# Optimization experiments

Measured on AMD Instinct MI355X. Metric: run time of the kernel, lower is better.

Reference implementation:

```python
import jax, jax.numpy as jnp
import numpy as np

B, T, D, DI, K, M, H, HD, L, VOCAB = 8, 512, 256, 512, 4, 2, 4, 64, 2, 272


def rmsnorm(x, w, eps=1e-6):
    return x * jax.lax.rsqrt(jnp.mean(x * x, axis=-1, keepdims=True) + eps) * w


def rotate_half(x):
    x1, x2 = x[..., ::2], x[..., 1::2]
    return jnp.stack([-x2, x1], axis=-1).reshape(x.shape)


def causal_conv(x, w, b):
    # x: [B,T,C], w: [C,K] depthwise causal conv, then silu
    y = jax.lax.conv_general_dilated(
        x.transpose(0, 2, 1), w[:, None, :],
        window_strides=(1,), padding=[(K - 1, 0)],
        feature_group_count=x.shape[-1])
    return jax.nn.silu(y.transpose(0, 2, 1) + b)


def delta_memory(x, Wv, Wg, Wb, Wa, A_log, dt_bias, Wblend, Wout):
    # x: [B,T,D]; per-timestep delta-rule fast-weight update with decay + key rotation
    Bv, Tn, Dm = x.shape
    vals = (x @ Wv).reshape(Bv, Tn, M, H, HD)
    gate = jax.nn.sigmoid(x @ Wg)                                   # [B,T,H]
    beta = jax.nn.sigmoid(jnp.einsum('btd,mdh->btmh', x, Wb))       # [B,T,M,H]
    alpha = jnp.einsum('btd,mdh->btmh', x, Wa) + dt_bias            # [B,T,M,H]
    decay = jnp.exp(-jnp.exp(A_log)[None, None] * jax.nn.softplus(alpha))
    blend = jax.nn.softmax((x @ Wblend).reshape(Bv, Tn, H, M), axis=-1)
    rk0 = x.reshape(Bv, Tn, H, HD)
    rk0 = rk0 / jnp.maximum(jnp.linalg.norm(rk0, axis=-1, keepdims=True), 1e-12)
    rks = [rk0]
    for _ in range(M - 1):
        rks.append(rotate_half(rks[-1]))
    rks = jnp.stack(rks, axis=2)                                    # [B,T,M,H,d]
    wks = jnp.pad(rks[:, :-1], ((0, 0), (1, 0), (0, 0), (0, 0), (0, 0)))  # shifted keys

    def step(S, inp):
        v, wk, rk, bt, dc, bl, g = inp
        S = S * dc[..., None, None]                                  # [B,M,H,d,d]
        pred = jnp.einsum('bmhdk,bmhd->bmhk', S, wk)
        err = (v - pred) * bt[..., None]
        S = S + wk[..., None] * err[..., None, :]                    # outer-product write
        read = jnp.einsum('bmhdk,bmhd->bmhk', S, rk)
        o = jnp.einsum('bhm,bmhk->bhk', bl, read) * g[..., None]
        return S, o

    tf = lambda a: jnp.moveaxis(a, 1, 0)
    xs = (tf(vals), tf(wks), tf(rks), tf(beta), tf(decay), tf(blend), tf(gate))
    S0 = jnp.zeros((Bv, M, H, HD, HD), x.dtype)
    _, o = jax.lax.scan(step, S0, xs)                                # [T,B,H,d]
    o = jnp.moveaxis(o, 0, 1).reshape(Bv, Tn, Dm)
    return x + o @ Wout


def setup_inputs():
    key = jax.random.key(0)
    ks = jax.random.split(key, 16)
    n = lambda k, shape, sc=0.02: jax.random.normal(k, shape, jnp.float32) * sc
    return {
        'ids': jax.random.randint(ks[0], (B, T), 0, VOCAB, jnp.int32),
        'emb': n(ks[1], (VOCAB, D)),
        'norm_w': jnp.ones((L, D), jnp.float32),
        'W_up': n(ks[2], (L, D, DI)),
        'W_gate': n(ks[3], (L, D, DI)),
        'W_down': n(ks[4], (L, DI, D)),
        'conv_w': n(ks[5], (L, DI, K), 0.1),
        'conv_b': jnp.zeros((L, DI), jnp.float32),
        'Wv': n(ks[6], (L, D, M * D)),
        'Wg': n(ks[7], (L, D, H)),
        'Wb': n(ks[8], (L, M, D, H)),
        'Wa': n(ks[9], (L, M, D, H)),
        'A_log': n(ks[10], (L, M, H), 0.5),
        'dt_bias': n(ks[11], (L, M, H), 0.5),
        'Wblend': n(ks[12], (L, D, H * M)),
        'Wout': n(ks[13], (L, D, D)),
        'final_norm_w': jnp.ones((D,), jnp.float32),
    }


def reference(ids, emb, norm_w, W_up, W_gate, W_down, conv_w, conv_b,
              Wv, Wg, Wb, Wa, A_log, dt_bias, Wblend, Wout, final_norm_w):
    x = emb[ids]
    for l in range(L):
        nx = rmsnorm(x, norm_w[l])
        h = causal_conv(nx @ W_up[l], conv_w[l], conv_b[l])
        out = (jax.nn.silu(nx @ W_gate[l]) * h) @ W_down[l]
        out = delta_memory(out, Wv[l], Wg[l], Wb[l], Wa[l],
                           A_log[l], dt_bias[l], Wblend[l], Wout[l])
        x = x + out
    return rmsnorm(x, final_norm_w) @ emb.T  # tied head
```

## Files before the change

kernel.cpp:

```cpp
#include <hip/hip_runtime.h>
#include <math.h>

#define BB 8
#define TT 512
#define DD 256
#define DIM 512
#define KW 4
#define MM 2
#define HH 4
#define HDIM 64
#define LL 2
#define VV 272

typedef __attribute__((ext_vector_type(8))) short bf16x8;
typedef __attribute__((ext_vector_type(4))) float f32x4;

__device__ __forceinline__ float sigf(float x){ return 1.f/(1.f+__expf(-x)); }
__device__ __forceinline__ float siluf(float x){ return x/(1.f+__expf(-x)); }

__device__ __forceinline__ unsigned short f2bf(float f){
  unsigned int u = __float_as_uint(f);
  unsigned int r = (u + 0x7FFFu + ((u >> 16) & 1u)) >> 16;
  return (unsigned short)r;
}
__device__ __forceinline__ float bf2f(unsigned short s){
  return __uint_as_float(((unsigned int)s) << 16);
}

__device__ __forceinline__ float xor1_add(float x){
  int y = __builtin_amdgcn_update_dpp(0, __float_as_int(x), 0xB1, 0xF, 0xF, true);
  return x + __int_as_float(y);
}
__device__ __forceinline__ float xor2_add(float x){
  int y = __builtin_amdgcn_update_dpp(0, __float_as_int(x), 0x4E, 0xF, 0xF, true);
  return x + __int_as_float(y);
}
__device__ __forceinline__ float ror4_add(float x){
  int y = __builtin_amdgcn_update_dpp(0, __float_as_int(x), 0x124, 0xF, 0xF, true);
  return x + __int_as_float(y);
}
__device__ __forceinline__ float ror8_add(float x){
  int y = __builtin_amdgcn_update_dpp(0, __float_as_int(x), 0x128, 0xF, 0xF, true);
  return x + __int_as_float(y);
}

__device__ __forceinline__ void gl_lds16(const void* g, void* l){
  __builtin_amdgcn_global_load_lds(
      (const __attribute__((address_space(1))) unsigned int*)g,
      (__attribute__((address_space(3))) unsigned int*)l,
      16, 0, 0);
}

#define LWB 589824
__global__ void k_cvt(const float* __restrict__ Wup, const float* __restrict__ Wgate,
                      const float* __restrict__ Wdown, const float* __restrict__ Wv,
                      const float* __restrict__ Wout, const float* __restrict__ emb,
                      unsigned short* __restrict__ wbf){
  int idx = blockIdx.x*256 + threadIdx.x;
  if (idx >= 2*LWB + VV*DD) return;
  float v;
  if (idx < 2*LWB){
    int l = (idx >= LWB) ? 1 : 0;
    int local = idx - l*LWB;
    if (local < 131072){ int n = local>>8, k = local&255;
      v = Wup[(size_t)l*131072 + k*DIM + n]; }
    else if (local < 262144){ local -= 131072; int n = local>>8, k = local&255;
      v = Wgate[(size_t)l*131072 + k*DIM + n]; }
    else if (local < 393216){ local -= 262144; int n = local>>9, k = local&511;
      v = Wdown[(size_t)l*131072 + k*DD + n]; }
    else if (local < 524288){ local -= 393216; int n = local>>8, k = local&255;
      v = Wv[(size_t)l*131072 + k*DIM + n]; }
    else { local -= 524288; int n = local>>8, k = local&255;
      v = Wout[(size_t)l*65536 + k*DD + n]; }
  } else {
    v = emb[idx - 2*LWB];
  }
  wbf[idx] = f2bf(v);
}

__global__ void __launch_bounds__(256) k_embed_norm(const int* __restrict__ ids,
                                                    const float* __restrict__ emb,
                                                    const float* __restrict__ w,
                                                    float* __restrict__ x,
                                                    unsigned short* __restrict__ out){
  const int wv = threadIdx.x >> 6, l = threadIdx.x & 63;
  const int row = blockIdx.x*4 + wv;
  float4 v = *(const float4*)&emb[(size_t)ids[row]*DD + l*4];
  *(float4*)&x[(size_t)row*DD + l*4] = v;
  float ss = v.x*v.x + v.y*v.y + v.z*v.z + v.w*v.w;
  #pragma unroll
  for (int o = 32; o > 0; o >>= 1) ss += __shfl_xor(ss, o, 64);
  float sc = rsqrtf(ss*(1.f/DD) + 1e-6f);
  float4 wvv = *(const float4*)&w[l*4];
  ushort4 r;
  r.x = f2bf(v.x*sc*wvv.x); r.y = f2bf(v.y*sc*wvv.y);
  r.z = f2bf(v.z*sc*wvv.z); r.w = f2bf(v.w*sc*wvv.w);
  *(ushort4*)&out[(size_t)row*DD + l*4] = r;
}

__global__ void __launch_bounds__(256) k_rmsnorm(const float* __restrict__ in,
                                                 const float* __restrict__ w,
                                                 unsigned short* __restrict__ out){
  const int wv = threadIdx.x >> 6, l = threadIdx.x & 63;
  const int row = blockIdx.x*4 + wv;
  float4 v = *(const float4*)&in[(size_t)row*DD + l*4];
  float ss = v.x*v.x + v.y*v.y + v.z*v.z + v.w*v.w;
  #pragma unroll
  for (int o = 32; o > 0; o >>= 1) ss += __shfl_xor(ss, o, 64);
  float sc = rsqrtf(ss*(1.f/DD) + 1e-6f);
  float4 wvv = *(const float4*)&w[l*4];
  ushort4 r;
  r.x = f2bf(v.x*sc*wvv.x); r.y = f2bf(v.y*sc*wvv.y);
  r.z = f2bf(v.z*sc*wvv.z); r.w = f2bf(v.w*sc*wvv.w);
  *(ushort4*)&out[(size_t)row*DD + l*4] = r;
}

template<int MODE>
__global__ void __launch_bounds__(256) k_gemm64(const unsigned short* __restrict__ A,
                                                const unsigned short* __restrict__ Bt,
                                                float* __restrict__ Cf,
                                                unsigned short* __restrict__ Cb,
                                                int N, int K){
  __shared__ unsigned short as[64][72];
  __shared__ unsigned short bs[64][72];
  const int tid = threadIdx.x;
  const int w = tid >> 6, l = tid & 63;
  const int m0 = blockIdx.y*64, n0 = blockIdx.x*64;
  const int ar = tid >> 2, ac = (tid & 3)*16;
  f32x4 acc[4] = {};
  for (int k0 = 0; k0 < K; k0 += 64){
    { const bf16x8* src = (const bf16x8*)&A[(size_t)(m0+ar)*K + k0 + ac];
      *(bf16x8*)&as[ar][ac]   = src[0];
      *(bf16x8*)&as[ar][ac+8] = src[1];
    }
    { int n = n0 + ar;
      bf16x8 z; z = (bf16x8)(short)0;
      bf16x8 b0 = z, b1 = z;
      if (n < N){
        const bf16x8* src = (const bf16x8*)&Bt[(size_t)n*K + k0 + ac];
        b0 = src[0]; b1 = src[1];
      }
      *(bf16x8*)&bs[ar][ac]   = b0;
      *(bf16x8*)&bs[ar][ac+8] = b1;
    }
    __syncthreads();
    const int mr = w*16 + (l & 15);
    const int kb = (l >> 4)*8;
    #pragma unroll
    for (int kc2 = 0; kc2 < 2; ++kc2){
      bf16x8 af = *(const bf16x8*)&as[mr][kc2*32 + kb];
      #pragma unroll
      for (int nt = 0; nt < 4; ++nt){
        bf16x8 bfr = *(const bf16x8*)&bs[nt*16 + (l & 15)][kc2*32 + kb];
        acc[nt] = __builtin_amdgcn_mfma_f32_16x16x32_bf16(af, bfr, acc[nt], 0, 0, 0);
      }
    }
    __syncthreads();
  }
  #pragma unroll
  for (int nt = 0; nt < 4; ++nt){
    int col = n0 + nt*16 + (l & 15);
    if (col < N){
      #pragma unroll
      for (int r = 0; r < 4; ++r){
        int row = m0 + w*16 + (l >> 4)*4 + r;
        if (MODE == 0 || MODE == 2) Cf[(size_t)row*N + col] = acc[nt][r];
        if (MODE == 1 || MODE == 2) Cb[(size_t)row*N + col] = f2bf(acc[nt][r]);
      }
    }
  }
}

template<int MODE>
__global__ void __launch_bounds__(256) k_gemm128(const unsigned short* __restrict__ A,
                                                 const unsigned short* __restrict__ Bt,
                                                 float* __restrict__ Cf,
                                                 unsigned short* __restrict__ Cb,
                                                 int N, int K){
  __shared__ unsigned short as[128][72];
  __shared__ unsigned short bs[64][72];
  const int tid = threadIdx.x;
  const int w = tid >> 6, l = tid & 63;
  const int m0 = blockIdx.y*128, n0 = blockIdx.x*64;
  const int ar = tid >> 1, ac = (tid & 1)*32;
  const int br = tid >> 2, bc = (tid & 3)*16;
  f32x4 acc[2][4] = {};
  for (int k0 = 0; k0 < K; k0 += 64){
    { const bf16x8* src = (const bf16x8*)&A[(size_t)(m0+ar)*K + k0 + ac];
      *(bf16x8*)&as[ar][ac]    = src[0];
      *(bf16x8*)&as[ar][ac+8]  = src[1];
      *(bf16x8*)&as[ar][ac+16] = src[2];
      *(bf16x8*)&as[ar][ac+24] = src[3];
    }
    { int n = n0 + br;
      bf16x8 z; z = (bf16x8)(short)0;
      bf16x8 b0 = z, b1 = z;
      if (n < N){
        const bf16x8* s = (const bf16x8*)&Bt[(size_t)n*K + k0 + bc];
        b0 = s[0]; b1 = s[1];
      }
      *(bf16x8*)&bs[br][bc]   = b0;
      *(bf16x8*)&bs[br][bc+8] = b1;
    }
    __syncthreads();
    const int lr = l & 15, kb = (l >> 4)*8;
    #pragma unroll
    for (int kc2 = 0; kc2 < 2; ++kc2){
      bf16x8 af0 = *(const bf16x8*)&as[w*32 + lr][kc2*32 + kb];
      bf16x8 af1 = *(const bf16x8*)&as[w*32 + 16 + lr][kc2*32 + kb];
      #pragma unroll
      for (int nt = 0; nt < 4; ++nt){
        bf16x8 bfr = *(const bf16x8*)&bs[nt*16 + lr][kc2*32 + kb];
        acc[0][nt] = __builtin_amdgcn_mfma_f32_16x16x32_bf16(af0, bfr, acc[0][nt], 0, 0, 0);
        acc[1][nt] = __builtin_amdgcn_mfma_f32_16x16x32_bf16(af1, bfr, acc[1][nt], 0, 0, 0);
      }
    }
    __syncthreads();
  }
  const int lr = l & 15;
  #pragma unroll
  for (int mt = 0; mt < 2; ++mt){
    #pragma unroll
    for (int nt = 0; nt < 4; ++nt){
      int col = n0 + nt*16 + lr;
      if (col < N){
        #pragma unroll
        for (int r = 0; r < 4; ++r){
          int row = m0 + w*32 + mt*16 + (l >> 4)*4 + r;
          if (MODE == 0 || MODE == 2) Cf[(size_t)row*N + col] = acc[mt][nt][r];
          if (MODE == 1 || MODE == 2) Cb[(size_t)row*N + col] = f2bf(acc[mt][nt][r]);
        }
      }
    }
  }
}

__global__ void __launch_bounds__(256) k_gemm_up(const unsigned short* __restrict__ A,
                                                 const unsigned short* __restrict__ But,
                                                 const unsigned short* __restrict__ Bgt,
                                                 unsigned short* __restrict__ Cu,
                                                 unsigned short* __restrict__ Cg){
  __shared__ unsigned short as[128][72];
  __shared__ unsigned short bu[64][72];
  __shared__ unsigned short bg[64][72];
  const int tid = threadIdx.x;
  const int w = tid >> 6, l = tid & 63;
  const int m0 = blockIdx.y*128, n0 = blockIdx.x*64;
  const int ar = tid >> 1, ac = (tid & 1)*32;
  const int br = tid >> 2, bc = (tid & 3)*16;
  f32x4 accu[2][4] = {}; f32x4 accg[2][4] = {};
  for (int k0 = 0; k0 < DD; k0 += 64){
    { const bf16x8* src = (const bf16x8*)&A[(size_t)(m0+ar)*DD + k0 + ac];
      *(bf16x8*)&as[ar][ac]    = src[0];
      *(bf16x8*)&as[ar][ac+8]  = src[1];
      *(bf16x8*)&as[ar][ac+16] = src[2];
      *(bf16x8*)&as[ar][ac+24] = src[3];
    }
    { const bf16x8* s0 = (const bf16x8*)&But[(size_t)(n0+br)*DD + k0 + bc];
      *(bf16x8*)&bu[br][bc]   = s0[0];
      *(bf16x8*)&bu[br][bc+8] = s0[1];
      const bf16x8* s1 = (const bf16x8*)&Bgt[(size_t)(n0+br)*DD + k0 + bc];
      *(bf16x8*)&bg[br][bc]   = s1[0];
      *(bf16x8*)&bg[br][bc+8] = s1[1];
    }
    __syncthreads();
    const int lr = l & 15, kb = (l >> 4)*8;
    #pragma unroll
    for (int kc2 = 0; kc2 < 2; ++kc2){
      bf16x8 af0 = *(const bf16x8*)&as[w*32 + lr][kc2*32 + kb];
      bf16x8 af1 = *(const bf16x8*)&as[w*32 + 16 + lr][kc2*32 + kb];
      #pragma unroll
      for (int nt = 0; nt < 4; ++nt){
        bf16x8 b0 = *(const bf16x8*)&bu[nt*16 + lr][kc2*32 + kb];
        accu[0][nt] = __builtin_amdgcn_mfma_f32_16x16x32_bf16(af0, b0, accu[0][nt], 0, 0, 0);
        accu[1][nt] = __builtin_amdgcn_mfma_f32_16x16x32_bf16(af1, b0, accu[1][nt], 0, 0, 0);
        bf16x8 b1 = *(const bf16x8*)&bg[nt*16 + lr][kc2*32 + kb];
        accg[0][nt] = __builtin_amdgcn_mfma_f32_16x16x32_bf16(af0, b1, accg[0][nt], 0, 0, 0);
        accg[1][nt] = __builtin_amdgcn_mfma_f32_16x16x32_bf16(af1, b1, accg[1][nt], 0, 0, 0);
      }
    }
    __syncthreads();
  }
  const int lr = l & 15;
  #pragma unroll
  for (int mt = 0; mt < 2; ++mt){
    #pragma unroll
    for (int nt = 0; nt < 4; ++nt){
      int col = n0 + nt*16 + lr;
      #pragma unroll
      for (int r = 0; r < 4; ++r){
        int row = m0 + w*32 + mt*16 + (l >> 4)*4 + r;
        Cu[(size_t)row*DIM + col] = f2bf(accu[mt][nt][r]);
        Cg[(size_t)row*DIM + col] = f2bf(accg[mt][nt][r]);
      }
    }
  }
}

__global__ void __launch_bounds__(256) k_gemm_wout(const float* __restrict__ p0,
                                                   const float* __restrict__ p1,
                                                   const unsigned short* __restrict__ Bt,
                                                   const float* __restrict__ y,
                                                   float* __restrict__ x){
  __shared__ unsigned short as[64][72];
  __shared__ unsigned short bs[64][72];
  const int tid = threadIdx.x;
  const int w = tid >> 6, l = tid & 63;
  const int m0 = blockIdx.y*64, n0 = blockIdx.x*64;
  const int ar = tid >> 2, ac = (tid & 3)*16;
  f32x4 acc[4] = {};
  for (int k0 = 0; k0 < DD; k0 += 64){
    #pragma unroll
    for (int j = 0; j < 4; ++j){
      size_t off = (size_t)(m0+ar)*DD + k0 + ac + j*4;
      float4 a = *(const float4*)&p0[off];
      float4 b = *(const float4*)&p1[off];
      a.x += b.x; a.y += b.y; a.z += b.z; a.w += b.w;
      ushort4 u = make_ushort4(f2bf(a.x), f2bf(a.y), f2bf(a.z), f2bf(a.w));
      *(ushort4*)&as[ar][ac + j*4] = u;
    }
    { const bf16x8* src = (const bf16x8*)&Bt[(size_t)(n0+ar)*DD + k0 + ac];
      *(bf16x8*)&bs[ar][ac]   = src[0];
      *(bf16x8*)&bs[ar][ac+8] = src[1];
    }
    __syncthreads();
    const int mr = w*16 + (l & 15);
    const int kb = (l >> 4)*8;
    #pragma unroll
    for (int kc2 = 0; kc2 < 2; ++kc2){
      bf16x8 af = *(const bf16x8*)&as[mr][kc2*32 + kb];
      #pragma unroll
      for (int nt = 0; nt < 4; ++nt){
        bf16x8 bfr = *(const bf16x8*)&bs[nt*16 + (l & 15)][kc2*32 + kb];
        acc[nt] = __builtin_amdgcn_mfma_f32_16x16x32_bf16(af, bfr, acc[nt], 0, 0, 0);
      }
    }
    __syncthreads();
  }
  #pragma unroll
  for (int nt = 0; nt < 4; ++nt){
    int col = n0 + nt*16 + (l & 15);
    #pragma unroll
    for (int r = 0; r < 4; ++r){
      int row = m0 + w*16 + (l >> 4)*4 + r;
      size_t off = (size_t)row*DD + col;
      x[off] = x[off] + y[off] + acc[nt][r];
    }
  }
}

__global__ void k_conv(const unsigned short* __restrict__ u,
                       const unsigned short* __restrict__ g,
                       const float* __restrict__ cw, const float* __restrict__ cb,
                       unsigned short* __restrict__ hh){
  int i8 = blockIdx.x*256 + threadIdx.x;
  int cg = i8 & 63;
  int bt = i8 >> 6;
  int t  = bt & (TT-1);
  int c0 = cg*8;
  float acc[8];
  { float4 b0 = *(const float4*)&cb[c0];
    float4 b1 = *(const float4*)&cb[c0+4];
    acc[0]=b0.x; acc[1]=b0.y; acc[2]=b0.z; acc[3]=b0.w;
    acc[4]=b1.x; acc[5]=b1.y; acc[6]=b1.z; acc[7]=b1.w; }
  float wts[8][4];
  #pragma unroll
  for (int i = 0; i < 8; ++i) *(float4*)&wts[i][0] = *(const float4*)&cw[(c0+i)*KW];
  #pragma unroll
  for (int j = 0; j < KW; ++j){
    int dt_ = j - (KW-1);
    if (t + dt_ >= 0){
      bf16x8 uv = *(const bf16x8*)&u[(size_t)(bt + dt_)*DIM + c0];
      #pragma unroll
      for (int i = 0; i < 8; ++i)
        acc[i] = fmaf(bf2f((unsigned short)uv[i]), wts[i][j], acc[i]);
    }
  }
  bf16x8 gv = *(const bf16x8*)&g[(size_t)bt*DIM + c0];
  bf16x8 o;
  #pragma unroll
  for (int i = 0; i < 8; ++i){
    float h = siluf(acc[i]);
    o[i] = (short)f2bf(siluf(bf2f((unsigned short)gv[i])) * h);
  }
  *(bf16x8*)&hh[(size_t)bt*DIM + c0] = o;
}

__global__ void __launch_bounds__(256) k_fused(const float* __restrict__ y,
    const float* __restrict__ Wg, const float* __restrict__ Wb,
    const float* __restrict__ Wa, const float* __restrict__ Wbl,
    const float* __restrict__ A_log, const float* __restrict__ dtb,
    float* __restrict__ rkb, float* __restrict__ scal){
  __shared__ float s_y[4][260];
  __shared__ float s_p[4][32];
  const int wv = threadIdx.x >> 6, l = threadIdx.x & 63;
  const int row = blockIdx.x*4 + wv;

  float4 yv = *(const float4*)&y[(size_t)row*DD + l*4];
  *(float4*)&s_y[wv][l*4] = yv;

  float ss = yv.x*yv.x + yv.y*yv.y + yv.z*yv.z + yv.w*yv.w;
  ss = xor1_add(ss); ss = xor2_add(ss);
  ss = ror4_add(ss); ss = ror8_add(ss);
  float inv = 1.f / fmaxf(sqrtf(ss), 1e-12f);
  float4 rv; rv.x = yv.x*inv; rv.y = yv.y*inv; rv.z = yv.z*inv; rv.w = yv.w*inv;
  *(float4*)&rkb[(size_t)row*DD + l*4] = rv;

  __syncthreads();

  const int j = (l < 28) ? l : 27;
  const float* wp; int stride;
  if (j < 4){ wp = Wg + j; stride = HH; }
  else if (j < 12){ int m=(j-4)>>2, h=(j-4)&3; wp = Wb + (size_t)m*DD*HH + h; stride = HH; }
  else if (j < 20){ int m=(j-12)>>2, h=(j-12)&3; wp = Wa + (size_t)m*DD*HH + h; stride = HH; }
  else { wp = Wbl + (j-20); stride = HH*MM; }
  float a0=0.f,a1=0.f,a2=0.f,a3=0.f;
  #pragma unroll 4
  for (int k = 0; k < DD; k += 4){
    a0 = fmaf(s_y[wv][k+0], wp[(k+0)*stride], a0);
    a1 = fmaf(s_y[wv][k+1], wp[(k+1)*stride], a1);
    a2 = fmaf(s_y[wv][k+2], wp[(k+2)*stride], a2);
    a3 = fmaf(s_y[wv][k+3], wp[(k+3)*stride], a3);
  }
  if (l < 28) s_p[wv][l] = (a0+a1)+(a2+a3);

  __syncthreads();

  if (l < 8){
    int m = l >> 2, h = l & 3;
    float gs  = sigf(s_p[wv][h]);
    float btv = sigf(s_p[wv][4 + m*4 + h]);
    float sp  = s_p[wv][12 + m*4 + h] + dtb[m*HH + h];
    sp = (sp > 15.f) ? sp : log1pf(__expf(sp));
    float dc  = __expf(-__expf(A_log[m*HH + h]) * sp);
    float l0 = s_p[wv][20 + h*2], l1 = s_p[wv][20 + h*2 + 1];
    float mx = fmaxf(l0, l1);
    float e0 = __expf(l0-mx), e1 = __expf(l1-mx);
    float bl = (m ? e1 : e0) / (e0 + e1);
    float4 o; o.x = dc; o.y = btv; o.z = bl*gs; o.w = 0.f;
    *(float4*)&scal[((size_t)row*MM + m)*(HH*4) + h*4] = o;
  }
}


#define SSTEP(T_, WK, RK, PF, VB, SB) { \
  const float dc = SB.x, btv = SB.y, blg = SB.z; \
  const float v = VB; \
  { const int tn_ = ((T_)+2 < 64) ? (T_)+2 : 63; \
    PF = *(const float4*)&s_rk[p][tn_][dbase]; \
    VB = bf2f(s_v[p][tn_][vidx]); \
    SB = *(const float4*)&s_sc[p][tn_][0]; } \
  const float err = (v - dc*rrc)*btv; \
  float rr0=0.f, rr1=0.f; \
  { const float4 rp = WK; const float4 rc = RK; \
    float w0,w1,w2,w3,c0,c1,c2,c3; \
    if (ROT == 0){ w0=rp.x; w1=rp.y; w2=rp.z; w3=rp.w; c0=rc.x; c1=rc.y; c2=rc.z; c3=rc.w; } \
    else { w0=-rp.y; w1=rp.x; w2=-rp.w; w3=rp.z; c0=-rc.y; c1=rc.x; c2=-rc.w; c3=rc.z; } \
    S[0] = fmaf(S[0], dc, w0*err); rr0 = fmaf(S[0], c0, rr0); \
    S[1] = fmaf(S[1], dc, w1*err); rr1 = fmaf(S[1], c1, rr1); \
    S[2] = fmaf(S[2], dc, w2*err); rr0 = fmaf(S[2], c2, rr0); \
    S[3] = fmaf(S[3], dc, w3*err); rr1 = fmaf(S[3], c3, rr1); } \
  float rr = rr0 + rr1; \
  rr = xor1_add(rr); rr = xor2_add(rr); rr = ror4_add(rr); rr = ror8_add(rr); \
  rrc = rr; \
  if (seg == 0) part[(size_t)(rowchunk + (T_))*DD + h*HDIM + kq4*4 + klocal] = blg*rr; \
}

template<int ROT>
__device__ __forceinline__ void scan_body(int b, int h, int kq4, int l,
    const unsigned short* __restrict__ vals, const float* __restrict__ rkb,
    const float* __restrict__ scal, float* __restrict__ part,
    float (*s_rk)[64][64], unsigned short (*s_v)[64][8], float (*s_sc)[64][4])
{
  const int seg = l & 15, klocal = l >> 4;
  const int dbase = seg*4;
  const int vidx = (kq4 & 1)*4 + klocal;
  const int kq8 = kq4 >> 1;
  const int rowbase = b*TT;

  float S[4];
  #pragma unroll
  for (int j = 0; j < 4; ++j) S[j] = 0.f;
  const float4 Z = make_float4(0.f,0.f,0.f,0.f);
  float4 rb0 = Z, rb1 = Z, rb2 = Z, rb3 = Z;
  float vb0 = 0.f, vb1 = 0.f;
  float4 sb0 = Z, sb1 = Z;
  float rrc = 0.f;

  auto stage = [&](int c, int pbuf){
    const int r0 = rowbase + c*64;
    #pragma unroll
    for (int i = 0; i < 16; ++i){
      const float* g = rkb + (size_t)(r0 + i*4 + (l>>4))*DD + h*HDIM + (l&15)*4;
      gl_lds16(g, &s_rk[pbuf][i*4][0]);
    }
    { const unsigned short* g = vals + ((size_t)(r0 + l)*MM + ROT)*DD + h*HDIM + kq8*8;
      gl_lds16(g, &s_v[pbuf][0][0]); }
    { const float* g = scal + ((size_t)(r0 + l)*MM + ROT)*(HH*4) + h*4;
      gl_lds16(g, &s_sc[pbuf][0][0]); }
  };

  stage(0, 0);
  for (int c = 0; c < TT/64; ++c){
    const int p = c & 1;
    __syncthreads();
    if (c + 1 < TT/64) stage(c+1, p^1);
    rb0 = *(const float4*)&s_rk[p][0][dbase];
    rb1 = *(const float4*)&s_rk[p][1][dbase];
    vb0 = bf2f(s_v[p][0][vidx]); vb1 = bf2f(s_v[p][1][vidx]);
    sb0 = *(const float4*)&s_sc[p][0][0]; sb1 = *(const float4*)&s_sc[p][1][0];
    const int rowchunk = rowbase + c*64;
    for (int tt = 0; tt < 64; tt += 4){
      SSTEP(tt+0, rb3, rb0, rb2, vb0, sb0)
      SSTEP(tt+1, rb0, rb1, rb3, vb1, sb1)
      SSTEP(tt+2, rb1, rb2, rb0, vb0, sb0)
      SSTEP(tt+3, rb2, rb3, rb1, vb1, sb1)
    }
  }
}

__global__ void __launch_bounds__(64) k_scan(const unsigned short* __restrict__ vals,
                                             const float* __restrict__ rkb,
                                             const float* __restrict__ scal,
                                             float* __restrict__ partials){
  __shared__ float s_rk[2][64][64];
  __shared__ unsigned short s_v[2][64][8];
  __shared__ float s_sc[2][64][4];
  const int bi = blockIdx.x;
  const int kq4 = bi & 15;
  const int m  = (bi >> 4) & 1;
  const int h  = (bi >> 5) & 3;
  const int b  = bi >> 7;
  float* part = partials + (size_t)m*(BB*TT*DD);
  if (m == 0) scan_body<0>(b, h, kq4, threadIdx.x, vals, rkb, scal, part, s_rk, s_v, s_sc);
  else        scan_body<1>(b, h, kq4, threadIdx.x, vals, rkb, scal, part, s_rk, s_v, s_sc);
}

extern "C" void kernel_launch(void* const* d_in, const int* in_sizes, int n_in,
                              void* d_out, int out_size, void* d_ws, size_t ws_size,
                              hipStream_t stream){
  const int*   ids   = (const int*)d_in[0];
  const float* emb   = (const float*)d_in[1];
  const float* normw = (const float*)d_in[2];
  const float* Wup   = (const float*)d_in[3];
  const float* Wgate = (const float*)d_in[4];
  const float* Wdown = (const float*)d_in[5];
  const float* convw = (const float*)d_in[6];
  const float* convb = (const float*)d_in[7];
  const float* Wv    = (const float*)d_in[8];
  const float* Wg    = (const float*)d_in[9];
  const float* Wb    = (const float*)d_in[10];
  const float* Wa    = (const float*)d_in[11];
  const float* A_log = (const float*)d_in[12];
  const float* dtb   = (const float*)d_in[13];
  const float* Wbl   = (const float*)d_in[14];
  const float* Wout  = (const float*)d_in[15];
  const float* fnw   = (const float*)d_in[16];
  float* out = (float*)d_out;

  const int ROWS = BB*TT;
  const size_t MEG = 1u << 20;
  float* ws   = (float*)d_ws;
  float* x    = ws;
  unsigned short* nyb = (unsigned short*)(x + MEG);
  float* big1 = x + MEG + MEG/2;
  float* big2 = big1 + 2*MEG;
  float* y    = big2 + 2*MEG;
  float* rkb  = y    + MEG;
  float* scal = rkb  + MEG;
  unsigned short* wbf = (unsigned short*)(scal + (1u<<17));

  unsigned short* ub  = (unsigned short*)big1;
  unsigned short* gb  = (unsigned short*)(big1 + MEG);
  unsigned short* valsb = ub;

  { int total = 2*LWB + VV*DD;
    k_cvt<<<(total + 255)/256, 256, 0, stream>>>(Wup, Wgate, Wdown, Wv, Wout, emb, wbf); }

  k_embed_norm<<<ROWS/4, 256, 0, stream>>>(ids, emb, normw, x, nyb);

  for (int l = 0; l < LL; ++l){
    unsigned short* wl = wbf + (size_t)l*LWB;
    unsigned short* upT   = wl;
    unsigned short* gateT = wl + 131072;
    unsigned short* downT = wl + 262144;
    unsigned short* wvT   = wl + 393216;
    unsigned short* woutT = wl + 524288;

    if (l > 0) k_rmsnorm<<<ROWS/4, 256, 0, stream>>>(x, normw + l*DD, nyb);
    k_gemm_up<<<dim3(DIM/64, ROWS/128), 256, 0, stream>>>(nyb, upT, gateT, ub, gb);
    k_conv<<<(ROWS*DIM/8)/256, 256, 0, stream>>>(ub, gb, convw + l*DIM*KW, convb + l*DIM, gb);
    k_gemm64<2><<<dim3(DD/64, ROWS/64), 256, 0, stream>>>(gb, downT, y, nyb, DD, DIM);
    k_gemm128<1><<<dim3(DIM/64, ROWS/128), 256, 0, stream>>>(nyb, wvT, nullptr, valsb, DIM, DD);
    k_fused<<<ROWS/4, 256, 0, stream>>>(y, Wg + l*DD*HH, Wb + (size_t)l*MM*DD*HH,
                                        Wa + (size_t)l*MM*DD*HH, Wbl + l*DD*HH*MM,
                                        A_log + l*MM*HH, dtb + l*MM*HH, rkb, scal);
    k_scan<<<BB*HH*MM*16, 64, 0, stream>>>(valsb, rkb, scal, big2);
    k_gemm_wout<<<dim3(DD/64, ROWS/64), 256, 0, stream>>>(big2, big2 + MEG, woutT, y, x);
  }

  unsigned short* embT = wbf + 2*LWB;
  k_rmsnorm<<<ROWS/4, 256, 0, stream>>>(x, fnw, nyb);
  k_gemm64<0><<<dim3((VV+63)/64, ROWS/64), 256, 0, stream>>>(nyb, embT, out, nullptr, VV, DD);
}
```

Measured before the change: 287.5 us.

## Break scan reduction dependency using precomputed key inner products

Adds a kernel that precomputes inner products between each rotated key and the keys one and two steps earlier. The scan uses these to rewrite the recurrence so that the read value for step t comes from err times a known inner product plus a term computed one step ahead. This takes the cross-lane DPP reduction off the serial critical path between consecutive timesteps. The cost is an extra kernel launch, more LDS staging and more per-step arithmetic, and the regrouped sums may change floating-point rounding.

```diff
diff --git a/kernel.cpp b/kernel.cpp
--- a/kernel.cpp
+++ b/kernel.cpp
@@ -11,6 +11,7 @@
 #define HDIM 64
 #define LL 2
 #define VV 272
+#define RP (BB*TT + 128)
 
 typedef __attribute__((ext_vector_type(8))) short bf16x8;
 typedef __attribute__((ext_vector_type(4))) float f32x4;
@@ -442,20 +443,43 @@
   }
 }
 
-
-#define SSTEP(T_, WK, RK, PF, VB, SB) { \
+__global__ void __launch_bounds__(256) k_ip(const float* __restrict__ rkb,
+                                            float* __restrict__ ipg){
+  const int wv = threadIdx.x >> 6, l = threadIdx.x & 63;
+  const int row = blockIdx.x*4 + wv;
+  const int t = row & (TT-1);
+  float4 a = *(const float4*)&rkb[(size_t)row*DD + l*4];
+  float4 b1 = make_float4(0.f,0.f,0.f,0.f), b2 = b1;
+  if (t >= 1) b1 = *(const float4*)&rkb[(size_t)(row-1)*DD + l*4];
+  if (t >= 2) b2 = *(const float4*)&rkb[(size_t)(row-2)*DD + l*4];
+  float p1 = a.x*b1.x; p1 = fmaf(a.y,b1.y,p1); p1 = fmaf(a.z,b1.z,p1); p1 = fmaf(a.w,b1.w,p1);
+  float p2 = a.x*b2.x; p2 = fmaf(a.y,b2.y,p2); p2 = fmaf(a.z,b2.z,p2); p2 = fmaf(a.w,b2.w,p2);
+  p1 = xor1_add(p1); p1 = xor2_add(p1); p1 = ror4_add(p1); p1 = ror8_add(p1);
+  p2 = xor1_add(p2); p2 = xor2_add(p2); p2 = ror4_add(p2); p2 = ror8_add(p2);
+  if ((l & 15) == 0){
+    int h = l >> 4;
+    float2 o; o.x = p1; o.y = p2;
+    *(float2*)&ipg[((size_t)h*RP + row)*2] = o;
+  }
+}
+
+
+#define WIRE(d0,d1,d2,d3, src) \
+  float d0,d1,d2,d3; \
+  if (ROT == 0){ d0=src.x; d1=src.y; d2=src.z; d3=src.w; } \
+  else { d0=-src.y; d1=src.x; d2=-src.w; d3=src.z; }
+
+#define BSTEP(T_, WK, RK, PF, VB, SB, IPB, ERRO, DCO) { \
   const float dc = SB.x, btv = SB.y, blg = SB.z; \
   const float v = VB; \
-  { const int tn_ = ((T_)+2 < 64) ? (T_)+2 : 63; \
+  { const int tn_ = (T_)+2; \
     PF = *(const float4*)&s_rk[p][tn_][dbase]; \
     VB = bf2f(s_v[p][tn_][vidx]); \
-    SB = *(const float4*)&s_sc[p][tn_][0]; } \
+    SB = *(const float4*)&s_sc[p][tn_][0]; \
+    IPB = *(const float2*)&s_ip[p][tn_][0]; } \
   const float err = (v - dc*rrc)*btv; \
   float rr0=0.f, rr1=0.f; \
-  { const float4 rp = WK; const float4 rc = RK; \
-    float w0,w1,w2,w3,c0,c1,c2,c3; \
-    if (ROT == 0){ w0=rp.x; w1=rp.y; w2=rp.z; w3=rp.w; c0=rc.x; c1=rc.y; c2=rc.z; c3=rc.w; } \
-    else { w0=-rp.y; w1=rp.x; w2=-rp.w; w3=rp.z; c0=-rc.y; c1=rc.x; c2=-rc.w; c3=rc.z; } \
+  { WIRE(w0,w1,w2,w3, WK) WIRE(c0,c1,c2,c3, RK) \
     S[0] = fmaf(S[0], dc, w0*err); rr0 = fmaf(S[0], c0, rr0); \
     S[1] = fmaf(S[1], dc, w1*err); rr1 = fmaf(S[1], c1, rr1); \
     S[2] = fmaf(S[2], dc, w2*err); rr0 = fmaf(S[2], c2, rr0); \
@@ -464,13 +488,51 @@
   rr = xor1_add(rr); rr = xor2_add(rr); rr = ror4_add(rr); rr = ror8_add(rr); \
   rrc = rr; \
   if (seg == 0) part[(size_t)(rowchunk + (T_))*DD + h*HDIM + kq4*4 + klocal] = blg*rr; \
+  ERRO = err; DCO = dc; \
+}
+
+#define FSTEP(T_, WK, RN, PF, VB, SB, IPB, SBo, IPBo) { \
+  const float dc = SB.x, btv = SB.y, blg = SB.z; \
+  const float ip1v = IPB.x; \
+  const float v = VB; \
+  const float dcN = SBo.x; \
+  const float ip2N = IPBo.y; \
+   \
+  float wv1; \
+  { WIRE(c0,c1,c2,c3, RN) \
+    float q0 = S[0]*c0; q0 = fmaf(S[2], c2, q0); \
+    float q1 = S[1]*c1; q1 = fmaf(S[3], c3, q1); \
+    wv1 = q0 + q1; } \
+   \
+  { const int tn_ = ((T_)+2 < 64) ? (T_)+2 : 63; \
+    PF = *(const float4*)&s_rk[p][tn_][dbase]; \
+    VB = bf2f(s_v[p][tn_][vidx]); \
+    SB = *(const float4*)&s_sc[p][tn_][0]; \
+    IPB = *(const float2*)&s_ip[p][tn_][0]; } \
+   \
+  const float err = (v - dc*rrc)*btv; \
+  const float rr = fmaf(err, ip1v, du); \
+  rrc = rr; \
+  if (seg == 0) part[(size_t)(rowchunk + (T_))*DD + h*HDIM + kq4*4 + klocal] = blg*rr; \
+   \
+  { WIRE(w0,w1,w2,w3, WK) \
+    S[0] = fmaf(S[0], dc, w0*err); \
+    S[1] = fmaf(S[1], dc, w1*err); \
+    S[2] = fmaf(S[2], dc, w2*err); \
+    S[3] = fmaf(S[3], dc, w3*err); } \
+   \
+  wv1 = xor1_add(wv1); wv1 = xor2_add(wv1); wv1 = ror4_add(wv1); wv1 = ror8_add(wv1); \
+  const float u1 = fmaf(err, ip2N, dc*wv1); \
+  du = dcN * u1; \
 }
 
 template<int ROT>
 __device__ __forceinline__ void scan_body(int b, int h, int kq4, int l,
     const unsigned short* __restrict__ vals, const float* __restrict__ rkb,
-    const float* __restrict__ scal, float* __restrict__ part,
-    float (*s_rk)[64][64], unsigned short (*s_v)[64][8], float (*s_sc)[64][4])
+    const float* __restrict__ scal, const float* __restrict__ ipg,
+    float* __restrict__ part,
+    float (*s_rk)[64][64], unsigned short (*s_v)[64][8], float (*s_sc)[64][4],
+    float (*s_ip)[128][2])
 {
   const int seg = l & 15, klocal = l >> 4;
   const int dbase = seg*4;
@@ -485,7 +547,9 @@
   float4 rb0 = Z, rb1 = Z, rb2 = Z, rb3 = Z;
   float vb0 = 0.f, vb1 = 0.f;
   float4 sb0 = Z, sb1 = Z;
+  float2 ipb0 = make_float2(0.f,0.f), ipb1 = ipb0;
   float rrc = 0.f;
+  float du = 0.f;
 
   auto stage = [&](int c, int pbuf){
     const int r0 = rowbase + c*64;
@@ -498,6 +562,8 @@
       gl_lds16(g, &s_v[pbuf][0][0]); }
     { const float* g = scal + ((size_t)(r0 + l)*MM + ROT)*(HH*4) + h*4;
       gl_lds16(g, &s_sc[pbuf][0][0]); }
+    { const float* g = ipg + ((size_t)h*RP + r0)*2 + l*4;
+      gl_lds16(g, &s_ip[pbuf][0][0]); }
   };
 
   stage(0, 0);
@@ -510,11 +576,26 @@
     vb0 = bf2f(s_v[p][0][vidx]); vb1 = bf2f(s_v[p][1][vidx]);
     sb0 = *(const float4*)&s_sc[p][0][0]; sb1 = *(const float4*)&s_sc[p][1][0];
     const int rowchunk = rowbase + c*64;
-    for (int tt = 0; tt < 64; tt += 4){
-      SSTEP(tt+0, rb3, rb0, rb2, vb0, sb0)
-      SSTEP(tt+1, rb0, rb1, rb3, vb1, sb1)
-      SSTEP(tt+2, rb1, rb2, rb0, vb0, sb0)
-      SSTEP(tt+3, rb2, rb3, rb1, vb1, sb1)
+
+    float err0, dc0d, err1, dc1d;
+    BSTEP(0, rb3, rb0, rb2, vb0, sb0, ipb0, err0, dc0d)
+    (void)err0; (void)dc0d;
+    float wv2;
+    { WIRE(c0,c1,c2,c3, rb2)
+      float q0 = S[0]*c0; q0 = fmaf(S[2], c2, q0);
+      float q1 = S[1]*c1; q1 = fmaf(S[3], c3, q1);
+      wv2 = q0 + q1;
+      wv2 = xor1_add(wv2); wv2 = xor2_add(wv2); wv2 = ror4_add(wv2); wv2 = ror8_add(wv2); }
+    BSTEP(1, rb0, rb1, rb3, vb1, sb1, ipb1, err1, dc1d)
+    { float u2 = fmaf(err1, ipb0.y, dc1d*wv2);
+      du = sb0.x * u2; }
+    FSTEP(2, rb1, rb3, rb0, vb0, sb0, ipb0, sb1, ipb1)
+    FSTEP(3, rb2, rb0, rb1, vb1, sb1, ipb1, sb0, ipb0)
+    for (int tt = 4; tt < 64; tt += 4){
+      FSTEP(tt+0, rb3, rb1, rb2, vb0, sb0, ipb0, sb1, ipb1)
+      FSTEP(tt+1, rb0, rb2, rb3, vb1, sb1, ipb1, sb0, ipb0)
+      FSTEP(tt+2, rb1, rb3, rb0, vb0, sb0, ipb0, sb1, ipb1)
+      FSTEP(tt+3, rb2, rb0, rb1, vb1, sb1, ipb1, sb0, ipb0)
     }
   }
 }
@@ -522,18 +603,20 @@
 __global__ void __launch_bounds__(64) k_scan(const unsigned short* __restrict__ vals,
                                              const float* __restrict__ rkb,
                                              const float* __restrict__ scal,
+                                             const float* __restrict__ ipg,
                                              float* __restrict__ partials){
   __shared__ float s_rk[2][64][64];
   __shared__ unsigned short s_v[2][64][8];
   __shared__ float s_sc[2][64][4];
+  __shared__ float s_ip[2][128][2];
   const int bi = blockIdx.x;
   const int kq4 = bi & 15;
   const int m  = (bi >> 4) & 1;
   const int h  = (bi >> 5) & 3;
   const int b  = bi >> 7;
   float* part = partials + (size_t)m*(BB*TT*DD);
-  if (m == 0) scan_body<0>(b, h, kq4, threadIdx.x, vals, rkb, scal, part, s_rk, s_v, s_sc);
-  else        scan_body<1>(b, h, kq4, threadIdx.x, vals, rkb, scal, part, s_rk, s_v, s_sc);
+  if (m == 0) scan_body<0>(b, h, kq4, threadIdx.x, vals, rkb, scal, ipg, part, s_rk, s_v, s_sc, s_ip);
+  else        scan_body<1>(b, h, kq4, threadIdx.x, vals, rkb, scal, ipg, part, s_rk, s_v, s_sc, s_ip);
 }
 
 extern "C" void kernel_launch(void* const* d_in, const int* in_sizes, int n_in,
@@ -568,7 +651,8 @@
   float* y    = big2 + 2*MEG;
   float* rkb  = y    + MEG;
   float* scal = rkb  + MEG;
-  unsigned short* wbf = (unsigned short*)(scal + (1u<<17));
+  float* ipg  = scal + (1u<<17);
+  unsigned short* wbf = (unsigned short*)(ipg + (size_t)HH*RP*2 + 256);
 
   unsigned short* ub  = (unsigned short*)big1;
   unsigned short* gb  = (unsigned short*)(big1 + MEG);
@@ -595,7 +679,8 @@
     k_fused<<<ROWS/4, 256, 0, stream>>>(y, Wg + l*DD*HH, Wb + (size_t)l*MM*DD*HH,
                                         Wa + (size_t)l*MM*DD*HH, Wbl + l*DD*HH*MM,
                                         A_log + l*MM*HH, dtb + l*MM*HH, rkb, scal);
-    k_scan<<<BB*HH*MM*16, 64, 0, stream>>>(valsb, rkb, scal, big2);
+    k_ip<<<ROWS/4, 256, 0, stream>>>(rkb, ipg);
+    k_scan<<<BB*HH*MM*16, 64, 0, stream>>>(valsb, rkb, scal, ipg, big2);
     k_gemm_wout<<<dim3(DD/64, ROWS/64), 256, 0, stream>>>(big2, big2 + MEG, woutT, y, x);
   }
 
```

After: 296.8 us. +3.2%, slower.

## Fuse RMSNorm into Wout epilogue and consumer GEMMs via partial row sums

Applied to the files above, without the earlier changes.

Removes the standalone rmsnorm kernels for layer 1 and the final norm. The Wout GEMM epilogue now writes per-column-block partial sums of squares for each row. The up/gate and logit GEMMs read fp32 x, apply the rsqrt scale while staging into LDS, and get the norm weights pre-folded into the bf16 weights during conversion. This saves two launches and an intermediate bf16 round trip, at the cost of fp32 A-operand loads and conversion inside the GEMM loads.

```diff
diff --git a/kernel.cpp b/kernel.cpp
--- a/kernel.cpp
+++ b/kernel.cpp
@@ -55,6 +55,7 @@
 __global__ void k_cvt(const float* __restrict__ Wup, const float* __restrict__ Wgate,
                       const float* __restrict__ Wdown, const float* __restrict__ Wv,
                       const float* __restrict__ Wout, const float* __restrict__ emb,
+                      const float* __restrict__ normw, const float* __restrict__ fnw,
                       unsigned short* __restrict__ wbf){
   int idx = blockIdx.x*256 + threadIdx.x;
   if (idx >= 2*LWB + VV*DD) return;
@@ -63,9 +64,11 @@
     int l = (idx >= LWB) ? 1 : 0;
     int local = idx - l*LWB;
     if (local < 131072){ int n = local>>8, k = local&255;
-      v = Wup[(size_t)l*131072 + k*DIM + n]; }
+      v = Wup[(size_t)l*131072 + k*DIM + n];
+      if (l == 1) v *= normw[DD + k]; }
     else if (local < 262144){ local -= 131072; int n = local>>8, k = local&255;
-      v = Wgate[(size_t)l*131072 + k*DIM + n]; }
+      v = Wgate[(size_t)l*131072 + k*DIM + n];
+      if (l == 1) v *= normw[DD + k]; }
     else if (local < 393216){ local -= 262144; int n = local>>9, k = local&511;
       v = Wdown[(size_t)l*131072 + k*DD + n]; }
     else if (local < 524288){ local -= 393216; int n = local>>8, k = local&255;
@@ -73,7 +76,8 @@
     else { local -= 524288; int n = local>>8, k = local&255;
       v = Wout[(size_t)l*65536 + k*DD + n]; }
   } else {
-    v = emb[idx - 2*LWB];
+    int k = (idx - 2*LWB) & 255;
+    v = emb[idx - 2*LWB] * fnw[k];
   }
   wbf[idx] = f2bf(v);
 }
@@ -87,23 +91,6 @@
   const int row = blockIdx.x*4 + wv;
   float4 v = *(const float4*)&emb[(size_t)ids[row]*DD + l*4];
   *(float4*)&x[(size_t)row*DD + l*4] = v;
-  float ss = v.x*v.x + v.y*v.y + v.z*v.z + v.w*v.w;
-  #pragma unroll
-  for (int o = 32; o > 0; o >>= 1) ss += __shfl_xor(ss, o, 64);
-  float sc = rsqrtf(ss*(1.f/DD) + 1e-6f);
-  float4 wvv = *(const float4*)&w[l*4];
-  ushort4 r;
-  r.x = f2bf(v.x*sc*wvv.x); r.y = f2bf(v.y*sc*wvv.y);
-  r.z = f2bf(v.z*sc*wvv.z); r.w = f2bf(v.w*sc*wvv.w);
-  *(ushort4*)&out[(size_t)row*DD + l*4] = r;
-}
-
-__global__ void __launch_bounds__(256) k_rmsnorm(const float* __restrict__ in,
-                                                 const float* __restrict__ w,
-                                                 unsigned short* __restrict__ out){
-  const int wv = threadIdx.x >> 6, l = threadIdx.x & 63;
-  const int row = blockIdx.x*4 + wv;
-  float4 v = *(const float4*)&in[(size_t)row*DD + l*4];
   float ss = v.x*v.x + v.y*v.y + v.z*v.z + v.w*v.w;
   #pragma unroll
   for (int o = 32; o > 0; o >>= 1) ss += __shfl_xor(ss, o, 64);
@@ -166,6 +153,68 @@
         int row = m0 + w*16 + (l >> 4)*4 + r;
         if (MODE == 0 || MODE == 2) Cf[(size_t)row*N + col] = acc[nt][r];
         if (MODE == 1 || MODE == 2) Cb[(size_t)row*N + col] = f2bf(acc[nt][r]);
+      }
+    }
+  }
+}
+
+__global__ void __launch_bounds__(256) k_gemmlogit(const float* __restrict__ X,
+                                                   const float* __restrict__ pssq,
+                                                   const unsigned short* __restrict__ Bt,
+                                                   float* __restrict__ Cf,
+                                                   int N, int K){
+  __shared__ unsigned short as[64][72];
+  __shared__ unsigned short bs[64][72];
+  const int tid = threadIdx.x;
+  const int w = tid >> 6, l = tid & 63;
+  const int m0 = blockIdx.y*64, n0 = blockIdx.x*64;
+  const int ar = tid >> 2, ac = (tid & 3)*16;
+  const int arow = m0 + ar;
+  const int ROWS = BB*TT;
+  float ssq = pssq[arow] + pssq[ROWS + arow] + pssq[2*ROWS + arow] + pssq[3*ROWS + arow];
+  const float sc = rsqrtf(ssq*(1.f/DD) + 1e-6f);
+  f32x4 acc[4] = {};
+  for (int k0 = 0; k0 < K; k0 += 64){
+    { const float* src = &X[(size_t)arow*K + k0 + ac];
+      #pragma unroll
+      for (int j = 0; j < 4; ++j){
+        float4 a = *(const float4*)&src[j*4];
+        ushort4 u = make_ushort4(f2bf(a.x*sc), f2bf(a.y*sc), f2bf(a.z*sc), f2bf(a.w*sc));
+        *(ushort4*)&as[ar][ac + j*4] = u;
+      }
+    }
+    { int n = n0 + ar;
+      bf16x8 z; z = (bf16x8)(short)0;
+      bf16x8 b0 = z, b1 = z;
+      if (n < N){
+        const bf16x8* src = (const bf16x8*)&Bt[(size_t)n*K + k0 + ac];
+        b0 = src[0]; b1 = src[1];
+      }
+      *(bf16x8*)&bs[ar][ac]   = b0;
+      *(bf16x8*)&bs[ar][ac+8] = b1;
+    }
+    __syncthreads();
+    const int mr = w*16 + (l & 15);
+    const int kb = (l >> 4)*8;
+    #pragma unroll
+    for (int kc2 = 0; kc2 < 2; ++kc2){
+      bf16x8 af = *(const bf16x8*)&as[mr][kc2*32 + kb];
+      #pragma unroll
+      for (int nt = 0; nt < 4; ++nt){
+        bf16x8 bfr = *(const bf16x8*)&bs[nt*16 + (l & 15)][kc2*32 + kb];
+        acc[nt] = __builtin_amdgcn_mfma_f32_16x16x32_bf16(af, bfr, acc[nt], 0, 0, 0);
+      }
+    }
+    __syncthreads();
+  }
+  #pragma unroll
+  for (int nt = 0; nt < 4; ++nt){
+    int col = n0 + nt*16 + (l & 15);
+    if (col < N){
+      #pragma unroll
+      for (int r = 0; r < 4; ++r){
+        int row = m0 + w*16 + (l >> 4)*4 + r;
+        Cf[(size_t)row*N + col] = acc[nt][r];
       }
     }
   }
@@ -297,11 +346,81 @@
   }
 }
 
+__global__ void __launch_bounds__(256) k_gemm_up2(const float* __restrict__ X,
+                                                  const float* __restrict__ pssq,
+                                                  const unsigned short* __restrict__ But,
+                                                  const unsigned short* __restrict__ Bgt,
+                                                  unsigned short* __restrict__ Cu,
+                                                  unsigned short* __restrict__ Cg){
+  __shared__ unsigned short as[128][72];
+  __shared__ unsigned short bu[64][72];
+  __shared__ unsigned short bg[64][72];
+  const int tid = threadIdx.x;
+  const int w = tid >> 6, l = tid & 63;
+  const int m0 = blockIdx.y*128, n0 = blockIdx.x*64;
+  const int ar = tid >> 1, ac = (tid & 1)*32;
+  const int br = tid >> 2, bc = (tid & 3)*16;
+  const int arow = m0 + ar;
+  const int ROWS = BB*TT;
+  float ssq = pssq[arow] + pssq[ROWS + arow] + pssq[2*ROWS + arow] + pssq[3*ROWS + arow];
+  const float sc = rsqrtf(ssq*(1.f/DD) + 1e-6f);
+  f32x4 accu[2][4] = {}; f32x4 accg[2][4] = {};
+  for (int k0 = 0; k0 < DD; k0 += 64){
+    { const float* src = &X[(size_t)arow*DD + k0 + ac];
+      #pragma unroll
+      for (int j = 0; j < 8; ++j){
+        float4 a = *(const float4*)&src[j*4];
+        ushort4 u = make_ushort4(f2bf(a.x*sc), f2bf(a.y*sc), f2bf(a.z*sc), f2bf(a.w*sc));
+        *(ushort4*)&as[ar][ac + j*4] = u;
+      }
+    }
+    { const bf16x8* s0 = (const bf16x8*)&But[(size_t)(n0+br)*DD + k0 + bc];
+      *(bf16x8*)&bu[br][bc]   = s0[0];
+      *(bf16x8*)&bu[br][bc+8] = s0[1];
+      const bf16x8* s1 = (const bf16x8*)&Bgt[(size_t)(n0+br)*DD + k0 + bc];
+      *(bf16x8*)&bg[br][bc]   = s1[0];
+      *(bf16x8*)&bg[br][bc+8] = s1[1];
+    }
+    __syncthreads();
+    const int lr = l & 15, kb = (l >> 4)*8;
+    #pragma unroll
+    for (int kc2 = 0; kc2 < 2; ++kc2){
+      bf16x8 af0 = *(const bf16x8*)&as[w*32 + lr][kc2*32 + kb];
+      bf16x8 af1 = *(const bf16x8*)&as[w*32 + 16 + lr][kc2*32 + kb];
+      #pragma unroll
+      for (int nt = 0; nt < 4; ++nt){
+        bf16x8 b0 = *(const bf16x8*)&bu[nt*16 + lr][kc2*32 + kb];
+        accu[0][nt] = __builtin_amdgcn_mfma_f32_16x16x32_bf16(af0, b0, accu[0][nt], 0, 0, 0);
+        accu[1][nt] = __builtin_amdgcn_mfma_f32_16x16x32_bf16(af1, b0, accu[1][nt], 0, 0, 0);
+        bf16x8 b1 = *(const bf16x8*)&bg[nt*16 + lr][kc2*32 + kb];
+        accg[0][nt] = __builtin_amdgcn_mfma_f32_16x16x32_bf16(af0, b1, accg[0][nt], 0, 0, 0);
+        accg[1][nt] = __builtin_amdgcn_mfma_f32_16x16x32_bf16(af1, b1, accg[1][nt], 0, 0, 0);
+      }
+    }
+    __syncthreads();
+  }
+  const int lr = l & 15;
+  #pragma unroll
+  for (int mt = 0; mt < 2; ++mt){
+    #pragma unroll
+    for (int nt = 0; nt < 4; ++nt){
+      int col = n0 + nt*16 + lr;
+      #pragma unroll
+      for (int r = 0; r < 4; ++r){
+        int row = m0 + w*32 + mt*16 + (l >> 4)*4 + r;
+        Cu[(size_t)row*DIM + col] = f2bf(accu[mt][nt][r]);
+        Cg[(size_t)row*DIM + col] = f2bf(accg[mt][nt][r]);
+      }
+    }
+  }
+}
+
 __global__ void __launch_bounds__(256) k_gemm_wout(const float* __restrict__ p0,
                                                    const float* __restrict__ p1,
                                                    const unsigned short* __restrict__ Bt,
                                                    const float* __restrict__ y,
-                                                   float* __restrict__ x){
+                                                   float* __restrict__ x,
+                                                   float* __restrict__ rowssq){
   __shared__ unsigned short as[64][72];
   __shared__ unsigned short bs[64][72];
   const int tid = threadIdx.x;
@@ -337,6 +456,8 @@
     }
     __syncthreads();
   }
+  const int ROWS = BB*TT;
+  float ssq[4] = {0.f, 0.f, 0.f, 0.f};
   #pragma unroll
   for (int nt = 0; nt < 4; ++nt){
     int col = n0 + nt*16 + (l & 15);
@@ -344,7 +465,18 @@
     for (int r = 0; r < 4; ++r){
       int row = m0 + w*16 + (l >> 4)*4 + r;
       size_t off = (size_t)row*DD + col;
-      x[off] = x[off] + y[off] + acc[nt][r];
+      float nv = x[off] + y[off] + acc[nt][r];
+      x[off] = nv;
+      ssq[r] = fmaf(nv, nv, ssq[r]);
+    }
+  }
+  #pragma unroll
+  for (int r = 0; r < 4; ++r){
+    float s = ssq[r];
+    s = xor1_add(s); s = xor2_add(s); s = ror4_add(s); s = ror8_add(s);
+    if ((l & 15) == 0){
+      int row = m0 + w*16 + (l >> 4)*4 + r;
+      rowssq[(size_t)blockIdx.x*ROWS + row] = s;
     }
   }
 }
@@ -441,7 +573,6 @@
     *(float4*)&scal[((size_t)row*MM + m)*(HH*4) + h*4] = o;
   }
 }
-
 
 #define SSTEP(T_, WK, RK, PF, VB, SB) { \
   const float dc = SB.x, btv = SB.y, blg = SB.z; \
@@ -568,14 +699,16 @@
   float* y    = big2 + 2*MEG;
   float* rkb  = y    + MEG;
   float* scal = rkb  + MEG;
-  unsigned short* wbf = (unsigned short*)(scal + (1u<<17));
+  float* rowssq = scal + (1u<<17);
+  unsigned short* wbf = (unsigned short*)(rowssq + 4*ROWS);
 
   unsigned short* ub  = (unsigned short*)big1;
   unsigned short* gb  = (unsigned short*)(big1 + MEG);
   unsigned short* valsb = ub;
 
   { int total = 2*LWB + VV*DD;
-    k_cvt<<<(total + 255)/256, 256, 0, stream>>>(Wup, Wgate, Wdown, Wv, Wout, emb, wbf); }
+    k_cvt<<<(total + 255)/256, 256, 0, stream>>>(Wup, Wgate, Wdown, Wv, Wout, emb,
+                                                 normw, fnw, wbf); }
 
   k_embed_norm<<<ROWS/4, 256, 0, stream>>>(ids, emb, normw, x, nyb);
 
@@ -587,8 +720,10 @@
     unsigned short* wvT   = wl + 393216;
     unsigned short* woutT = wl + 524288;
 
-    if (l > 0) k_rmsnorm<<<ROWS/4, 256, 0, stream>>>(x, normw + l*DD, nyb);
-    k_gemm_up<<<dim3(DIM/64, ROWS/128), 256, 0, stream>>>(nyb, upT, gateT, ub, gb);
+    if (l == 0)
+      k_gemm_up<<<dim3(DIM/64, ROWS/128), 256, 0, stream>>>(nyb, upT, gateT, ub, gb);
+    else
+      k_gemm_up2<<<dim3(DIM/64, ROWS/128), 256, 0, stream>>>(x, rowssq, upT, gateT, ub, gb);
     k_conv<<<(ROWS*DIM/8)/256, 256, 0, stream>>>(ub, gb, convw + l*DIM*KW, convb + l*DIM, gb);
     k_gemm64<2><<<dim3(DD/64, ROWS/64), 256, 0, stream>>>(gb, downT, y, nyb, DD, DIM);
     k_gemm128<1><<<dim3(DIM/64, ROWS/128), 256, 0, stream>>>(nyb, wvT, nullptr, valsb, DIM, DD);
@@ -596,10 +731,9 @@
                                         Wa + (size_t)l*MM*DD*HH, Wbl + l*DD*HH*MM,
                                         A_log + l*MM*HH, dtb + l*MM*HH, rkb, scal);
     k_scan<<<BB*HH*MM*16, 64, 0, stream>>>(valsb, rkb, scal, big2);
-    k_gemm_wout<<<dim3(DD/64, ROWS/64), 256, 0, stream>>>(big2, big2 + MEG, woutT, y, x);
+    k_gemm_wout<<<dim3(DD/64, ROWS/64), 256, 0, stream>>>(big2, big2 + MEG, woutT, y, x, rowssq);
   }
 
   unsigned short* embT = wbf + 2*LWB;
-  k_rmsnorm<<<ROWS/4, 256, 0, stream>>>(x, fnw, nyb);
-  k_gemm64<0><<<dim3((VV+63)/64, ROWS/64), 256, 0, stream>>>(nyb, embT, out, nullptr, VV, DD);
-}
+  k_gemmlogit<<<dim3((VV+63)/64, ROWS/64), 256, 0, stream>>>(x, rowssq, embT, out, VV, DD);
+}
```

After: 284.9 us. Within noise of the previous version (-0.9%).
